# Kernel tuning notes

Measured on AMD Instinct MI355X. Metric: run time of the kernel, lower is better.

## Reference

```python
import jax, jax.numpy as jnp
import numpy as np

B, L, D = 2, 4096, 1024
H = 8
DK = D // H          # 128 head qk dim (expand_k=1)
DV = 2 * D // H      # 256 head v dim (expand_v=2)
FFN = 4 * D          # 4096
CHUNK = 64
EPS = 1e-6


def _ln(x, w, b):
    mu = x.mean(-1, keepdims=True)
    var = ((x - mu) ** 2).mean(-1, keepdims=True)
    return (x - mu) / jnp.sqrt(var + EPS) * w + b


def _retention(q, k, v):
    # q,k: [B,H,L,DK], v: [B,H,L,DV]; RetNet decayed causal linear attention,
    # computed chunkwise (intra-chunk parallel + inter-chunk recurrent state).
    Bq, Hq, Lq, Dk = q.shape
    Dv = v.shape[-1]
    N = Lq // CHUNK
    b = 1.0 - jnp.exp2(-5.0 - jnp.arange(Hq, dtype=q.dtype))   # [H] per-head decay
    logb = jnp.log(b)
    q = q * (Dk ** -0.5)
    t = jnp.arange(CHUNK, dtype=q.dtype)
    diff = t[:, None] - t[None, :]                              # [C,C]
    mask = jnp.where(diff >= 0, jnp.exp(logb[:, None, None] * diff), 0.0)  # [H,C,C]
    d_q = jnp.exp(logb[:, None] * (t[None, :] + 1.0))           # b^(t+1), [H,C]
    d_k = jnp.exp(logb[:, None] * (CHUNK - 1.0 - t[None, :]))   # b^(C-1-s), [H,C]
    d_c = jnp.exp(logb * CHUNK)                                 # b^C, [H]

    def to_chunks(x):
        return x.reshape(Bq, Hq, N, CHUNK, -1).transpose(2, 0, 1, 3, 4)  # [N,B,H,C,d]

    qc, kc, vc = to_chunks(q), to_chunks(k), to_chunks(v)
    S0 = jnp.zeros((Bq, Hq, Dk, Dv), q.dtype)

    def step(S, inp):
        qi, ki, vi = inp                                        # [B,H,C,*]
        A = jnp.einsum('bhtd,bhsd->bhts', qi, ki) * mask        # intra-chunk scores
        o = jnp.einsum('bhts,bhsv->bhtv', A, vi)
        o = o + jnp.einsum('bhtd,bhdv->bhtv', qi * d_q[None, :, :, None], S)
        S = S * d_c[None, :, None, None] + jnp.einsum('bhsd,bhsv->bhdv', ki * d_k[None, :, :, None], vi)
        return S, o

    _, os = jax.lax.scan(step, S0, (qc, kc, vc))                # os: [N,B,H,C,DV]
    return os.transpose(1, 2, 0, 3, 4).reshape(Bq, Hq, Lq, Dv)


def setup_inputs() -> dict:
    key = jax.random.key(0)
    ks = jax.random.split(key, 8)
    s = 0.02
    return {
        'x': jax.random.normal(ks[0], (B, L, D), jnp.float32),
        'ln1_w': jnp.ones((D,), jnp.float32),
        'ln1_b': jnp.zeros((D,), jnp.float32),
        'Wq': jax.random.normal(ks[1], (D, D), jnp.float32) * s,
        'Wk': jax.random.normal(ks[2], (D, D), jnp.float32) * s,
        'Wv': jax.random.normal(ks[3], (D, 2 * D), jnp.float32) * s,
        'Wo': jax.random.normal(ks[4], (2 * D, D), jnp.float32) * s,
        'ln2_w': jnp.ones((D,), jnp.float32),
        'ln2_b': jnp.zeros((D,), jnp.float32),
        'W1': jax.random.normal(ks[5], (D, FFN), jnp.float32) * s,
        'b1': jnp.zeros((FFN,), jnp.float32),
        'W2': jax.random.normal(ks[6], (FFN, D), jnp.float32) * s,
        'b2': jnp.zeros((D,), jnp.float32),
    }


def reference(x, ln1_w, ln1_b, Wq, Wk, Wv, Wo, ln2_w, ln2_b, W1, b1, W2, b2):
    # retention branch
    h = _ln(x, ln1_w, ln1_b)
    q = (h @ Wq).reshape(B, L, H, DK).transpose(0, 2, 1, 3)
    k = (h @ Wk).reshape(B, L, H, DK).transpose(0, 2, 1, 3)
    v = (h @ Wv).reshape(B, L, H, DV).transpose(0, 2, 1, 3)
    o = _retention(q, k, v)                                      # [B,H,L,DV]
    o = o.transpose(0, 2, 1, 3).reshape(B, L, H * DV)
    x = x + o @ Wo
    # FFN branch (exact gelu, no subln, eval-mode dropout)
    f = _ln(x, ln2_w, ln2_b)
    f = jax.nn.gelu(f @ W1 + b1, approximate=False)
    x = x + (f @ W2 + b2)
    return x
```

## Files before the change

### kernel.cpp

```cpp
#include <hip/hip_runtime.h>
#include <math.h>

typedef short s16;
typedef __attribute__((ext_vector_type(8))) short short8;
typedef __attribute__((ext_vector_type(4))) float f32x4;

__device__ __forceinline__ float bf2f_lo(unsigned u){ return __builtin_bit_cast(float, u << 16); }
__device__ __forceinline__ float bf2f_hi(unsigned u){ return __builtin_bit_cast(float, u & 0xffff0000u); }
__device__ __forceinline__ float bf2f(unsigned short h){ return __builtin_bit_cast(float, (unsigned)h << 16); }
__device__ __forceinline__ s16 f2bf(float f){
  unsigned u = __builtin_bit_cast(unsigned, f);
  u += 0x7fffu + ((u >> 16) & 1u);
  return (s16)(u >> 16);
}
__device__ __forceinline__ void unpack8(int4 v, float* f){
  unsigned a=(unsigned)v.x, b=(unsigned)v.y, c=(unsigned)v.z, d=(unsigned)v.w;
  f[0]=bf2f_lo(a); f[1]=bf2f_hi(a); f[2]=bf2f_lo(b); f[3]=bf2f_hi(b);
  f[4]=bf2f_lo(c); f[5]=bf2f_hi(c); f[6]=bf2f_lo(d); f[7]=bf2f_hi(d);
}
__device__ __forceinline__ void gl2lds16(const s16* g, s16* l){
  __builtin_amdgcn_global_load_lds((const __attribute__((address_space(1))) void*)g,
                                   (__attribute__((address_space(3))) void*)l, 16, 0, 0);
}

__global__ __launch_bounds__(256) void ln_bf16(const float* __restrict__ x,
                                               const float* __restrict__ w,
                                               const float* __restrict__ b,
                                               s16* __restrict__ out){
  int row = blockIdx.x; int t = threadIdx.x;
  const float* xr = x + (size_t)row * 1024;
  float4 v = *(const float4*)(xr + t*4);
  float s = v.x + v.y + v.z + v.w;
  float ss = v.x*v.x + v.y*v.y + v.z*v.z + v.w*v.w;
  for (int o = 32; o > 0; o >>= 1){ s += __shfl_down(s, o, 64); ss += __shfl_down(ss, o, 64); }
  __shared__ float red[8];
  int wid = t >> 6, lane = t & 63;
  if (lane == 0){ red[wid] = s; red[4+wid] = ss; }
  __syncthreads();
  if (t == 0){
    float S = red[0]+red[1]+red[2]+red[3];
    float SS = red[4]+red[5]+red[6]+red[7];
    red[0] = S * (1.f/1024.f);
    red[1] = SS * (1.f/1024.f);
  }
  __syncthreads();
  float mu = red[0];
  float var = red[1] - mu*mu;
  float rstd = rsqrtf(var + 1e-6f);
  float vv[4] = {v.x, v.y, v.z, v.w};
  short4 o4;
  s16 tmp[4];
  #pragma unroll
  for (int i = 0; i < 4; ++i){
    int c = t*4 + i;
    float val = (vv[i] - mu) * rstd * w[c] + b[c];
    tmp[i] = f2bf(val);
  }
  o4.x = tmp[0]; o4.y = tmp[1]; o4.z = tmp[2]; o4.w = tmp[3];
  *(short4*)(out + (size_t)row*1024 + t*4) = o4;
}

__global__ __launch_bounds__(256) void conv_t(const float* __restrict__ W,
                                              s16* __restrict__ Wt,
                                              int K, int N, float scale){
  __shared__ float tile[32][33];
  int n0 = blockIdx.x * 32, k0 = blockIdx.y * 32;
  int tx = threadIdx.x & 31, ty = threadIdx.x >> 5;
  #pragma unroll
  for (int i = 0; i < 4; ++i){
    int r = ty + i*8;
    tile[r][tx] = W[(size_t)(k0 + r)*N + n0 + tx];
  }
  __syncthreads();
  #pragma unroll
  for (int i = 0; i < 4; ++i){
    int r = ty + i*8;
    Wt[(size_t)(n0 + r)*K + k0 + tx] = f2bf(tile[tx][r] * scale);
  }
}

__device__ __forceinline__ void xcd_tile(int tiles_y, int& tx, int& ty){
  int id = blockIdx.x;
  int sy = tiles_y >> 3;
  int xcd = id & 7, p = id >> 3;
  ty = xcd * sy + (p % sy);
  tx = p / sy;
}

__global__ __launch_bounds__(512,2) void gemm256(const s16* __restrict__ A,
                                                 const s16* __restrict__ Bt,
                                                 int N, int K,
                                                 s16* __restrict__ Cb,
                                                 const float* __restrict__ bias,
                                                 int flags, int tiles_y){
  __shared__ s16 lds[2*4*8192];
  int t = threadIdx.x;
  int tx, ty; xcd_tile(tiles_y, tx, ty);
  int m0 = ty * 256, n0 = tx * 256;
  int w = t >> 6, lane = t & 63;
  int wm = w >> 2, wn = w & 3;
  int lrow = lane & 15, lq = lane >> 4;
  int s = lrow & 7;

  int grow = t >> 3;
  int g = (t & 7) ^ (grow & 7);
  const s16* Ag = A  + (size_t)(m0 + grow) * K + g*8;
  const s16* Bg = Bt + (size_t)(n0 + grow) * K + g*8;
  int wo = w * 512;

  int abase = (wm*64 + lrow) * 64;
  int bbase = (wn*32 + lrow) * 64;
  int sw0 = ((lq ^ s) << 3);
  int sw1 = (((4 + lq) ^ s) << 3);

  f32x4 acc[2][4][2][2];
  #pragma unroll
  for (int a = 0; a < 2; ++a)
    #pragma unroll
    for (int b = 0; b < 4; ++b)
      #pragma unroll
      for (int c = 0; c < 2; ++c)
        #pragma unroll
        for (int d = 0; d < 2; ++d) acc[a][b][c][d] = (f32x4){0.f,0.f,0.f,0.f};

  short8 af[2][4];
  short8 bfr[2][2][2];

#define STG_A(buf,h,kt) do{ \
    gl2lds16(Ag + (size_t)((h)*128    )*K + (kt)*64, lds + ((buf)*4+(h))*8192 + wo); \
    gl2lds16(Ag + (size_t)((h)*128+ 64)*K + (kt)*64, lds + ((buf)*4+(h))*8192 + 4096 + wo); }while(0)
#define STG_B(buf,nh,kt) do{ \
    gl2lds16(Bg + (size_t)((nh)*128    )*K + (kt)*64, lds + ((buf)*4+2+(nh))*8192 + wo); \
    gl2lds16(Bg + (size_t)((nh)*128+ 64)*K + (kt)*64, lds + ((buf)*4+2+(nh))*8192 + 4096 + wo); }while(0)
#define RD_A(buf,mh) do{ const s16* p_ = lds + ((buf)*4+(mh))*8192 + abase; \
    _Pragma("unroll") for (int m_ = 0; m_ < 4; ++m_){ \
      af[0][m_] = *(const short8*)(p_ + m_*1024 + sw0); \
      af[1][m_] = *(const short8*)(p_ + m_*1024 + sw1); } }while(0)
#define RD_B(buf,nh) do{ const s16* p_ = lds + ((buf)*4+2+(nh))*8192 + bbase; \
    _Pragma("unroll") for (int n_ = 0; n_ < 2; ++n_){ \
      bfr[nh][0][n_] = *(const short8*)(p_ + n_*1024 + sw0); \
      bfr[nh][1][n_] = *(const short8*)(p_ + n_*1024 + sw1); } }while(0)
#define MFMA_Q(mh,nh) do{ __builtin_amdgcn_s_setprio(1); \
    _Pragma("unroll") for (int kk_ = 0; kk_ < 2; ++kk_) \
      _Pragma("unroll") for (int m_ = 0; m_ < 4; ++m_) \
        _Pragma("unroll") for (int n_ = 0; n_ < 2; ++n_) \
          acc[mh][m_][nh][n_] = __builtin_amdgcn_mfma_f32_16x16x32_bf16( \
              af[kk_][m_], bfr[nh][kk_][n_], acc[mh][m_][nh][n_], 0, 0, 0); \
    __builtin_amdgcn_s_setprio(0); }while(0)
#define VM6() asm volatile("s_waitcnt vmcnt(6)" ::: "memory")
#define BARR() asm volatile("s_barrier" ::: "memory")

  int NT = K >> 6;
  STG_A(0,0,0); STG_B(0,0,0); STG_B(0,1,0); STG_A(0,1,0);

  for (int kt = 0; kt < NT-1; ++kt){
    int cb = kt & 1, nb = cb ^ 1;
    STG_A(nb,0,kt+1);
    VM6(); BARR();
    RD_A(cb,0); RD_B(cb,0);
    MFMA_Q(0,0);
    BARR();
    STG_B(nb,0,kt+1);
    VM6(); BARR();
    RD_B(cb,1);
    MFMA_Q(0,1);
    BARR();
    STG_B(nb,1,kt+1);
    VM6(); BARR();
    RD_A(cb,1);
    MFMA_Q(1,0);
    BARR();
    STG_A(nb,1,kt+1);
    BARR();
    MFMA_Q(1,1);
    BARR();
  }
  {
    int cb = (NT-1) & 1;
    asm volatile("s_waitcnt vmcnt(4)" ::: "memory"); BARR();
    RD_A(cb,0); RD_B(cb,0); MFMA_Q(0,0); BARR();
    asm volatile("s_waitcnt vmcnt(2)" ::: "memory"); BARR();
    RD_B(cb,1); MFMA_Q(0,1); BARR();
    asm volatile("s_waitcnt vmcnt(0)" ::: "memory"); BARR();
    RD_A(cb,1); MFMA_Q(1,0); BARR();
    MFMA_Q(1,1);
  }
#undef STG_A
#undef STG_B
#undef RD_A
#undef RD_B
#undef MFMA_Q
#undef VM6
#undef BARR

  bool do_gelu = flags & 1;
  #pragma unroll
  for (int nh = 0; nh < 2; ++nh){
    #pragma unroll
    for (int nj = 0; nj < 2; ++nj){
      int col = n0 + wn*32 + nh*128 + nj*16 + lrow;
      float bcol = bias ? bias[col] : 0.f;
      #pragma unroll
      for (int mh = 0; mh < 2; ++mh){
        #pragma unroll
        for (int m = 0; m < 4; ++m){
          int row_base = m0 + wm*64 + mh*128 + m*16 + lq*4;
          #pragma unroll
          for (int r = 0; r < 4; ++r){
            float val = acc[mh][m][nh][nj][r] + bcol;
            if (do_gelu) val = 0.5f * val * (1.f + erff(val * 0.70710678118654752f));
            Cb[(size_t)(row_base + r) * N + col] = f2bf(val);
          }
        }
      }
    }
  }
}

__global__ __launch_bounds__(256,2) void gemm_nt_h(const s16* __restrict__ A,
                                                   const s16* __restrict__ Bt,
                                                   int M, int N, int K, int ldb,
                                                   float* __restrict__ Cf,
                                                   s16* __restrict__ Cb,
                                                   const float* __restrict__ bias,
                                                   const float* __restrict__ resid,
                                                   int flags, int tiles_y){
  __shared__ s16 As0[64*32], As1[64*32];
  __shared__ s16 Bs0[128*32], Bs1[128*32];
  int t = threadIdx.x;
  int tx, ty; xcd_tile(tiles_y, tx, ty);
  int m0 = ty * 64, n0 = tx * 128;
  int w = t >> 6, lane = t & 63;
  int lrow = lane & 15, lq = lane >> 4;
  f32x4 acc[4][2];
  #pragma unroll
  for (int i = 0; i < 4; ++i)
    #pragma unroll
    for (int j = 0; j < 2; ++j) acc[i][j] = (f32x4){0.f,0.f,0.f,0.f};

  const s16* Ag = A  + (size_t)(m0 + (t>>2)) * K   + (t&3)*8;
  const s16* Bg = Bt + (size_t)(n0 + (t>>2)) * ldb + (t&3)*8;
  int wo = w*512;

  for (int k0 = 0; k0 < K; k0 += 64){
    __syncthreads();
    gl2lds16(Ag + k0,      As0 + wo);
    gl2lds16(Ag + k0 + 32, As1 + wo);
    gl2lds16(Bg + k0,                       Bs0 + wo);
    gl2lds16(Bg + (size_t)64*ldb + k0,      Bs0 + 2048 + wo);
    gl2lds16(Bg + k0 + 32,                  Bs1 + wo);
    gl2lds16(Bg + (size_t)64*ldb + k0 + 32, Bs1 + 2048 + wo);
    __syncthreads();
    short8 af[4], bfr[2];
    #pragma unroll
    for (int mi = 0; mi < 4; ++mi)
      af[mi] = *(short8*)&As0[(mi*16 + lrow)*32 + lq*8];
    #pragma unroll
    for (int ni = 0; ni < 2; ++ni)
      bfr[ni] = *(short8*)&Bs0[(w*32 + ni*16 + lrow)*32 + lq*8];
    #pragma unroll
    for (int mi = 0; mi < 4; ++mi)
      #pragma unroll
      for (int ni = 0; ni < 2; ++ni)
        acc[mi][ni] = __builtin_amdgcn_mfma_f32_16x16x32_bf16(af[mi], bfr[ni], acc[mi][ni], 0, 0, 0);
    #pragma unroll
    for (int mi = 0; mi < 4; ++mi)
      af[mi] = *(short8*)&As1[(mi*16 + lrow)*32 + lq*8];
    #pragma unroll
    for (int ni = 0; ni < 2; ++ni)
      bfr[ni] = *(short8*)&Bs1[(w*32 + ni*16 + lrow)*32 + lq*8];
    #pragma unroll
    for (int mi = 0; mi < 4; ++mi)
      #pragma unroll
      for (int ni = 0; ni < 2; ++ni)
        acc[mi][ni] = __builtin_amdgcn_mfma_f32_16x16x32_bf16(af[mi], bfr[ni], acc[mi][ni], 0, 0, 0);
  }

  bool do_gelu = flags & 1;
  bool out_bf = flags & 2;
  #pragma unroll
  for (int mi = 0; mi < 4; ++mi){
    #pragma unroll
    for (int ni = 0; ni < 2; ++ni){
      int gcol = n0 + w*32 + ni*16 + lrow;
      float bcol = bias ? bias[gcol] : 0.f;
      int grow_base = m0 + mi*16 + lq*4;
      #pragma unroll
      for (int r = 0; r < 4; ++r){
        int grow = grow_base + r;
        float val = acc[mi][ni][r] + bcol;
        if (do_gelu) val = 0.5f * val * (1.f + erff(val * 0.70710678118654752f));
        if (resid) val += resid[(size_t)grow * N + gcol];
        if (out_bf) Cb[(size_t)grow * N + gcol] = f2bf(val);
        else        Cf[(size_t)grow * N + gcol] = val;
      }
    }
  }
}

__global__ __launch_bounds__(256,2) void ret_chunksum(const s16* __restrict__ k,
                                                      const s16* __restrict__ v,
                                                      s16* __restrict__ U){
  int bi = blockIdx.x;
  int h = bi & 7, n = bi >> 3;
  int t = threadIdx.x;
  __shared__ s16 ks[128*72];
  __shared__ s16 vs[256*72];
  float log2b = log2f(1.f - exp2f(-5.f - (float)h));
  const s16* kbase = k + (size_t)(n*64)*4096 + h*128;
  const s16* vbase = v + (size_t)(n*64)*4096 + h*256;
  #pragma unroll
  for (int i = 0; i < 4; ++i){
    int e = i*2048 + t*8;
    int s = e >> 7, dk = e & 127;
    int4 kv = *(const int4*)(kbase + (size_t)s*4096 + dk);
    float f[8]; unpack8(kv, f);
    float dec = exp2f(log2b * (float)(63 - s));
    #pragma unroll
    for (int j = 0; j < 8; ++j) ks[(dk+j)*72 + s] = f2bf(f[j]*dec);
  }
  #pragma unroll
  for (int i = 0; i < 8; ++i){
    int e = i*2048 + t*8;
    int s = e >> 8, dv = e & 255;
    int4 vv = *(const int4*)(vbase + (size_t)s*4096 + dv);
    s16 tmp[8]; *(int4*)tmp = vv;
    #pragma unroll
    for (int j = 0; j < 8; ++j) vs[(dv+j)*72 + s] = tmp[j];
  }
  __syncthreads();
  int w = t >> 6, lane = t & 63;
  int m0w = w*64;
  int lrow = lane & 15, lq = lane >> 4;
  f32x4 acc[4][8];
  #pragma unroll
  for (int mi = 0; mi < 4; ++mi)
    #pragma unroll
    for (int ni = 0; ni < 8; ++ni) acc[mi][ni] = (f32x4){0.f,0.f,0.f,0.f};
  #pragma unroll
  for (int kk = 0; kk < 64; kk += 32){
    short8 af[4], bfr[8];
    #pragma unroll
    for (int mi = 0; mi < 4; ++mi)
      af[mi] = *(short8*)&vs[(m0w + mi*16 + lrow)*72 + kk + lq*8];
    #pragma unroll
    for (int ni = 0; ni < 8; ++ni)
      bfr[ni] = *(short8*)&ks[(ni*16 + lrow)*72 + kk + lq*8];
    #pragma unroll
    for (int mi = 0; mi < 4; ++mi)
      #pragma unroll
      for (int ni = 0; ni < 8; ++ni)
        acc[mi][ni] = __builtin_amdgcn_mfma_f32_16x16x32_bf16(af[mi], bfr[ni], acc[mi][ni], 0, 0, 0);
  }
  s16* Ub = U + ((size_t)(h*64 + n))*32768;
  #pragma unroll
  for (int mi = 0; mi < 4; ++mi)
    #pragma unroll
    for (int ni = 0; ni < 8; ++ni)
      #pragma unroll
      for (int r = 0; r < 4; ++r){
        int row = m0w + mi*16 + lq*4 + r;
        int col = ni*16 + lrow;
        Ub[(size_t)row*128 + col] = f2bf(acc[mi][ni][r]);
      }
}

__global__ __launch_bounds__(256) void ret_scan(s16* __restrict__ US){
  int tid = blockIdx.x*256 + threadIdx.x;
  int h = tid >> 12;
  int rem = tid & 4095;
  int dv = rem >> 4, dk0 = (rem & 15)*8;
  float log2b = log2f(1.f - exp2f(-5.f - (float)h));
  float dc = exp2f(log2b * 64.f);
  s16* base = US + (size_t)h*64*32768 + (size_t)dv*128 + dk0;
  float acc[8] = {0.f,0.f,0.f,0.f,0.f,0.f,0.f,0.f};
  #pragma unroll 4
  for (int n = 0; n < 64; ++n){
    s16* p = base + (size_t)n*32768;
    int4 u4 = *(const int4*)p;
    float uf[8]; unpack8(u4, uf);
    s16 sb[8];
    #pragma unroll
    for (int j = 0; j < 8; ++j) sb[j] = f2bf(acc[j]);
    *(int4*)p = *(int4*)sb;
    #pragma unroll
    for (int j = 0; j < 8; ++j) acc[j] = acc[j]*dc + uf[j];
  }
}

__global__ __launch_bounds__(256,2) void ret_attn(const s16* __restrict__ q,
                                                  const s16* __restrict__ k,
                                                  const s16* __restrict__ v,
                                                  const s16* __restrict__ S,
                                                  s16* __restrict__ o){
  int bi = blockIdx.x;
  int h = bi & 7, n = bi >> 3;
  int t = threadIdx.x;
  int w = t >> 6, lane = t & 63;
  int lrow = lane & 15, lq = lane >> 4;
  float log2b = log2f(1.f - exp2f(-5.f - (float)h));
  __shared__ s16 As[64*72];
  __shared__ s16 vs[256*72];

  const s16* vbase = v + (size_t)(n*64)*4096 + h*256;
  #pragma unroll
  for (int i = 0; i < 8; ++i){
    int e = i*2048 + t*8;
    int s = e >> 8, dv = e & 255;
    int4 vv = *(const int4*)(vbase + (size_t)s*4096 + dv);
    s16 tmp[8]; *(int4*)tmp = vv;
    #pragma unroll
    for (int j = 0; j < 8; ++j) vs[(dv+j)*72 + s] = tmp[j];
  }

  const s16* qbase = q + (size_t)(n*64)*4096 + h*128;
  const s16* kbase = k + (size_t)(n*64)*4096 + h*128;
  short8 qf[4][4];
  #pragma unroll
  for (int ti = 0; ti < 4; ++ti)
    #pragma unroll
    for (int c = 0; c < 4; ++c)
      qf[ti][c] = *(const short8*)(qbase + (size_t)(ti*16 + lrow)*4096 + c*32 + lq*8);
  short8 kf[4];
  #pragma unroll
  for (int c = 0; c < 4; ++c)
    kf[c] = *(const short8*)(kbase + (size_t)(16*w + lrow)*4096 + c*32 + lq*8);
  #pragma unroll
  for (int ti = 0; ti < 4; ++ti){
    f32x4 acc_a = (f32x4){0.f,0.f,0.f,0.f};
    #pragma unroll
    for (int c = 0; c < 4; ++c)
      acc_a = __builtin_amdgcn_mfma_f32_16x16x32_bf16(qf[ti][c], kf[c], acc_a, 0, 0, 0);
    #pragma unroll
    for (int r = 0; r < 4; ++r){
      int ti_idx = ti*16 + lq*4 + r;
      int s_idx = 16*w + lrow;
      int d = ti_idx - s_idx;
      float val = (d >= 0) ? acc_a[r] * exp2f(log2b * (float)d) : 0.f;
      As[ti_idx*72 + s_idx] = f2bf(val);
    }
  }
  __syncthreads();

  f32x4 acc[4][4];
  #pragma unroll
  for (int mi = 0; mi < 4; ++mi)
    #pragma unroll
    for (int nj = 0; nj < 4; ++nj) acc[mi][nj] = (f32x4){0.f,0.f,0.f,0.f};

  const s16* Sbase = S + ((size_t)(h*64 + n)*256 + w*64)*128;
  #pragma unroll
  for (int c = 0; c < 4; ++c){
    short8 bf[4];
    #pragma unroll
    for (int nj = 0; nj < 4; ++nj)
      bf[nj] = *(const short8*)(Sbase + (size_t)(nj*16 + lrow)*128 + c*32 + lq*8);
    #pragma unroll
    for (int mi = 0; mi < 4; ++mi)
      #pragma unroll
      for (int nj = 0; nj < 4; ++nj)
        acc[mi][nj] = __builtin_amdgcn_mfma_f32_16x16x32_bf16(qf[mi][c], bf[nj], acc[mi][nj], 0, 0, 0);
  }
  #pragma unroll
  for (int mi = 0; mi < 4; ++mi){
    #pragma unroll
    for (int r = 0; r < 4; ++r){
      float dq = exp2f(log2b * (float)(mi*16 + lq*4 + r + 1));
      #pragma unroll
      for (int nj = 0; nj < 4; ++nj) acc[mi][nj][r] *= dq;
    }
  }
  #pragma unroll
  for (int c = 0; c < 2; ++c){
    short8 af[4], bf[4];
    #pragma unroll
    for (int mi = 0; mi < 4; ++mi)
      af[mi] = *(short8*)&As[(mi*16 + lrow)*72 + c*32 + lq*8];
    #pragma unroll
    for (int nj = 0; nj < 4; ++nj)
      bf[nj] = *(short8*)&vs[(w*64 + nj*16 + lrow)*72 + c*32 + lq*8];
    #pragma unroll
    for (int mi = 0; mi < 4; ++mi)
      #pragma unroll
      for (int nj = 0; nj < 4; ++nj)
        acc[mi][nj] = __builtin_amdgcn_mfma_f32_16x16x32_bf16(af[mi], bf[nj], acc[mi][nj], 0, 0, 0);
  }
  s16* obase = o + (size_t)(n*64)*2048 + h*256;
  #pragma unroll
  for (int mi = 0; mi < 4; ++mi)
    #pragma unroll
    for (int nj = 0; nj < 4; ++nj)
      #pragma unroll
      for (int r = 0; r < 4; ++r){
        int row = mi*16 + lq*4 + r;
        int col = w*64 + nj*16 + lrow;
        obase[(size_t)row*2048 + col] = f2bf(acc[mi][nj][r]);
      }
}

extern "C" void kernel_launch(void* const* d_in, const int* in_sizes, int n_in,
                              void* d_out, int out_size, void* d_ws, size_t ws_size,
                              hipStream_t stream) {
  (void)in_sizes; (void)n_in; (void)out_size; (void)ws_size;
  const float* x     = (const float*)d_in[0];
  const float* ln1_w = (const float*)d_in[1];
  const float* ln1_b = (const float*)d_in[2];
  const float* Wq    = (const float*)d_in[3];
  const float* Wk    = (const float*)d_in[4];
  const float* Wv    = (const float*)d_in[5];
  const float* Wo    = (const float*)d_in[6];
  const float* ln2_w = (const float*)d_in[7];
  const float* ln2_b = (const float*)d_in[8];
  const float* W1    = (const float*)d_in[9];
  const float* b1    = (const float*)d_in[10];
  const float* W2    = (const float*)d_in[11];
  const float* b2    = (const float*)d_in[12];
  float* out = (float*)d_out;
  char* ws = (char*)d_ws;

  const size_t MB = 1ull << 20;
  s16* Wqkv_t = (s16*)(ws + 0*MB);
  s16* Wo_t = (s16*)(ws + 8*MB);
  s16* W1_t = (s16*)(ws + 12*MB);
  s16* W2_t = (s16*)(ws + 20*MB);
  s16* hbuf = (s16*)(ws + 28*MB);
  s16* h2   = (s16*)(ws + 28*MB);
  s16* qkv  = (s16*)(ws + 44*MB);
  float* x1 = (float*)(ws + 44*MB);
  s16* fb   = (s16*)(ws + 76*MB);
  s16* US   = (s16*)(ws + 108*MB);
  s16* ob   = (s16*)(ws + 140*MB);

  conv_t<<<dim3(32,32),  256, 0, stream>>>(Wq, Wqkv_t, 1024, 1024, 0.08838834764831845f);
  conv_t<<<dim3(32,32),  256, 0, stream>>>(Wk, Wqkv_t + (size_t)1024*1024, 1024, 1024, 1.f);
  conv_t<<<dim3(64,32),  256, 0, stream>>>(Wv, Wqkv_t + (size_t)2048*1024, 1024, 2048, 1.f);
  conv_t<<<dim3(32,64),  256, 0, stream>>>(Wo, Wo_t, 2048, 1024, 1.f);
  conv_t<<<dim3(128,32), 256, 0, stream>>>(W1, W1_t, 1024, 4096, 1.f);
  conv_t<<<dim3(32,128), 256, 0, stream>>>(W2, W2_t, 4096, 1024, 1.f);

  ln_bf16<<<8192, 256, 0, stream>>>(x, ln1_w, ln1_b, hbuf);

  gemm256<<<512, 512, 0, stream>>>(hbuf, Wqkv_t, 4096, 1024, qkv, nullptr, 0, 32);

  for (int b = 0; b < 2; ++b){
    const s16* q_b = qkv + (size_t)b*4096*4096;
    const s16* k_b = q_b + 1024;
    const s16* v_b = q_b + 2048;
    s16* ob_b = ob + (size_t)b*4096*2048;
    ret_chunksum<<<512, 256, 0, stream>>>(k_b, v_b, US);
    ret_scan<<<128, 256, 0, stream>>>(US);
    ret_attn<<<512, 256, 0, stream>>>(q_b, k_b, v_b, US, ob_b);
  }

  gemm_nt_h<<<1024, 256, 0, stream>>>(ob, Wo_t, 8192, 1024, 2048, 2048, x1, nullptr, nullptr, x, 0, 128);
  ln_bf16<<<8192, 256, 0, stream>>>(x1, ln2_w, ln2_b, h2);

  gemm256<<<512, 512, 0, stream>>>(h2, W1_t, 4096, 1024, fb, b1, 1, 32);
  gemm_nt_h<<<1024, 256, 0, stream>>>(fb, W2_t, 8192, 1024, 4096, 4096, out, nullptr, b2, x1, 0, 128);
}
```

Measured before the change: 623.1 us.

## Deepen gemm256 prefetch pipeline and replace narrow-N GEMM with 256x128 pipelined kernel

The gemm256 main loop now prefetches two k-tiles ahead, issuing loads for the next-next tile into the buffer just consumed, so global-to-LDS latency overlaps more MFMA work. A new gemm256h kernel (256x128 tiles, 512 threads, swizzled LDS, same staged pipeline) replaces the small 64x128 gemm_nt_h for the Wo and W2 projections. The aim is higher data reuse and fewer launched blocks per output. The cost is more LDS per block and only 256 blocks, which may underfill the CUs.

```diff
diff --git a/kernel.cpp b/kernel.cpp
--- a/kernel.cpp
+++ b/kernel.cpp
@@ -86,6 +86,9 @@
   ty = xcd * sy + (p % sy);
   tx = p / sy;
 }
+
+#define VMW(n) asm volatile("s_waitcnt vmcnt(" #n ")" ::: "memory")
+#define BARR() asm volatile("s_barrier" ::: "memory")
 
 __global__ __launch_bounds__(512,2) void gemm256(const s16* __restrict__ A,
                                                  const s16* __restrict__ Bt,
@@ -147,42 +150,47 @@
           acc[mh][m_][nh][n_] = __builtin_amdgcn_mfma_f32_16x16x32_bf16( \
               af[kk_][m_], bfr[nh][kk_][n_], acc[mh][m_][nh][n_], 0, 0, 0); \
     __builtin_amdgcn_s_setprio(0); }while(0)
-#define VM6() asm volatile("s_waitcnt vmcnt(6)" ::: "memory")
-#define BARR() asm volatile("s_barrier" ::: "memory")
 
   int NT = K >> 6;
   STG_A(0,0,0); STG_B(0,0,0); STG_B(0,1,0); STG_A(0,1,0);
-
-  for (int kt = 0; kt < NT-1; ++kt){
+  STG_A(1,0,1); STG_B(1,0,1); STG_B(1,1,1);
+  VMW(6); BARR();
+
+  for (int kt = 0; kt < NT-2; ++kt){
     int cb = kt & 1, nb = cb ^ 1;
-    STG_A(nb,0,kt+1);
-    VM6(); BARR();
     RD_A(cb,0); RD_B(cb,0);
-    MFMA_Q(0,0);
-    BARR();
-    STG_B(nb,0,kt+1);
-    VM6(); BARR();
+    STG_A(nb,1,kt+1);
+    BARR(); MFMA_Q(0,0); BARR();
     RD_B(cb,1);
-    MFMA_Q(0,1);
-    BARR();
-    STG_B(nb,1,kt+1);
-    VM6(); BARR();
+    STG_A(cb,0,kt+2);
+    BARR(); MFMA_Q(0,1); BARR();
     RD_A(cb,1);
-    MFMA_Q(1,0);
-    BARR();
-    STG_A(nb,1,kt+1);
-    BARR();
-    MFMA_Q(1,1);
-    BARR();
+    STG_B(cb,0,kt+2);
+    BARR(); MFMA_Q(1,0); BARR();
+    STG_B(cb,1,kt+2);
+    VMW(6);
+    BARR(); MFMA_Q(1,1); BARR();
+  }
+  {
+    int cb = (NT-2) & 1, nb = cb ^ 1;
+    RD_A(cb,0); RD_B(cb,0);
+    STG_A(nb,1,NT-1);
+    BARR(); MFMA_Q(0,0); BARR();
+    RD_B(cb,1);
+    BARR(); MFMA_Q(0,1); BARR();
+    RD_A(cb,1);
+    BARR(); MFMA_Q(1,0); BARR();
+    VMW(0);
+    BARR(); MFMA_Q(1,1); BARR();
   }
   {
     int cb = (NT-1) & 1;
-    asm volatile("s_waitcnt vmcnt(4)" ::: "memory"); BARR();
-    RD_A(cb,0); RD_B(cb,0); MFMA_Q(0,0); BARR();
-    asm volatile("s_waitcnt vmcnt(2)" ::: "memory"); BARR();
-    RD_B(cb,1); MFMA_Q(0,1); BARR();
-    asm volatile("s_waitcnt vmcnt(0)" ::: "memory"); BARR();
-    RD_A(cb,1); MFMA_Q(1,0); BARR();
+    RD_A(cb,0); RD_B(cb,0);
+    BARR(); MFMA_Q(0,0); BARR();
+    RD_B(cb,1);
+    BARR(); MFMA_Q(0,1); BARR();
+    RD_A(cb,1);
+    BARR(); MFMA_Q(1,0); BARR();
     MFMA_Q(1,1);
   }
 #undef STG_A
@@ -190,8 +198,6 @@
 #undef RD_A
 #undef RD_B
 #undef MFMA_Q
-#undef VM6
-#undef BARR
 
   bool do_gelu = flags & 1;
   #pragma unroll
@@ -217,82 +223,123 @@
   }
 }
 
-__global__ __launch_bounds__(256,2) void gemm_nt_h(const s16* __restrict__ A,
-                                                   const s16* __restrict__ Bt,
-                                                   int M, int N, int K, int ldb,
-                                                   float* __restrict__ Cf,
-                                                   s16* __restrict__ Cb,
-                                                   const float* __restrict__ bias,
-                                                   const float* __restrict__ resid,
-                                                   int flags, int tiles_y){
-  __shared__ s16 As0[64*32], As1[64*32];
-  __shared__ s16 Bs0[128*32], Bs1[128*32];
+__global__ __launch_bounds__(512,2) void gemm256h(const s16* __restrict__ A,
+                                                  const s16* __restrict__ Bt,
+                                                  int N, int K,
+                                                  float* __restrict__ Cf,
+                                                  s16* __restrict__ Cb,
+                                                  const float* __restrict__ bias,
+                                                  const float* __restrict__ resid,
+                                                  int flags, int tiles_y){
+  __shared__ s16 lds[2*3*8192];
   int t = threadIdx.x;
   int tx, ty; xcd_tile(tiles_y, tx, ty);
-  int m0 = ty * 64, n0 = tx * 128;
+  int m0 = ty * 256, n0 = tx * 128;
   int w = t >> 6, lane = t & 63;
+  int wm = w >> 2, wn = w & 3;
   int lrow = lane & 15, lq = lane >> 4;
-  f32x4 acc[4][2];
-  #pragma unroll
-  for (int i = 0; i < 4; ++i)
-    #pragma unroll
-    for (int j = 0; j < 2; ++j) acc[i][j] = (f32x4){0.f,0.f,0.f,0.f};
-
-  const s16* Ag = A  + (size_t)(m0 + (t>>2)) * K   + (t&3)*8;
-  const s16* Bg = Bt + (size_t)(n0 + (t>>2)) * ldb + (t&3)*8;
-  int wo = w*512;
-
-  for (int k0 = 0; k0 < K; k0 += 64){
-    __syncthreads();
-    gl2lds16(Ag + k0,      As0 + wo);
-    gl2lds16(Ag + k0 + 32, As1 + wo);
-    gl2lds16(Bg + k0,                       Bs0 + wo);
-    gl2lds16(Bg + (size_t)64*ldb + k0,      Bs0 + 2048 + wo);
-    gl2lds16(Bg + k0 + 32,                  Bs1 + wo);
-    gl2lds16(Bg + (size_t)64*ldb + k0 + 32, Bs1 + 2048 + wo);
-    __syncthreads();
-    short8 af[4], bfr[2];
-    #pragma unroll
-    for (int mi = 0; mi < 4; ++mi)
-      af[mi] = *(short8*)&As0[(mi*16 + lrow)*32 + lq*8];
-    #pragma unroll
-    for (int ni = 0; ni < 2; ++ni)
-      bfr[ni] = *(short8*)&Bs0[(w*32 + ni*16 + lrow)*32 + lq*8];
-    #pragma unroll
-    for (int mi = 0; mi < 4; ++mi)
-      #pragma unroll
-      for (int ni = 0; ni < 2; ++ni)
-        acc[mi][ni] = __builtin_amdgcn_mfma_f32_16x16x32_bf16(af[mi], bfr[ni], acc[mi][ni], 0, 0, 0);
-    #pragma unroll
-    for (int mi = 0; mi < 4; ++mi)
-      af[mi] = *(short8*)&As1[(mi*16 + lrow)*32 + lq*8];
-    #pragma unroll
-    for (int ni = 0; ni < 2; ++ni)
-      bfr[ni] = *(short8*)&Bs1[(w*32 + ni*16 + lrow)*32 + lq*8];
-    #pragma unroll
-    for (int mi = 0; mi < 4; ++mi)
-      #pragma unroll
-      for (int ni = 0; ni < 2; ++ni)
-        acc[mi][ni] = __builtin_amdgcn_mfma_f32_16x16x32_bf16(af[mi], bfr[ni], acc[mi][ni], 0, 0, 0);
-  }
+  int s = lrow & 7;
+
+  int grow = t >> 3;
+  int g = (t & 7) ^ (grow & 7);
+  const s16* Ag = A  + (size_t)(m0 + grow) * K + g*8;
+  const s16* Bg = Bt + (size_t)(n0 + grow) * K + g*8;
+  int wo = w * 512;
+
+  int abase = (wm*64 + lrow) * 64;
+  int bbase = (wn*32 + lrow) * 64;
+  int sw0 = ((lq ^ s) << 3);
+  int sw1 = (((4 + lq) ^ s) << 3);
+
+  f32x4 acc[2][4][2];
+  #pragma unroll
+  for (int a = 0; a < 2; ++a)
+    #pragma unroll
+    for (int b = 0; b < 4; ++b)
+      #pragma unroll
+      for (int c = 0; c < 2; ++c) acc[a][b][c] = (f32x4){0.f,0.f,0.f,0.f};
+
+  short8 af[2][4], bfr[2][2];
+
+#define STG_A(buf,h,kt) do{ \
+    gl2lds16(Ag + (size_t)((h)*128    )*K + (kt)*64, lds + ((buf)*3+(h))*8192 + wo); \
+    gl2lds16(Ag + (size_t)((h)*128+ 64)*K + (kt)*64, lds + ((buf)*3+(h))*8192 + 4096 + wo); }while(0)
+#define STG_B(buf,kt) do{ \
+    gl2lds16(Bg + (size_t)0*K  + (kt)*64, lds + ((buf)*3+2)*8192 + wo); \
+    gl2lds16(Bg + (size_t)64*K + (kt)*64, lds + ((buf)*3+2)*8192 + 4096 + wo); }while(0)
+#define RD_A(buf,mh) do{ const s16* p_ = lds + ((buf)*3+(mh))*8192 + abase; \
+    _Pragma("unroll") for (int m_ = 0; m_ < 4; ++m_){ \
+      af[0][m_] = *(const short8*)(p_ + m_*1024 + sw0); \
+      af[1][m_] = *(const short8*)(p_ + m_*1024 + sw1); } }while(0)
+#define RD_B(buf) do{ const s16* p_ = lds + ((buf)*3+2)*8192 + bbase; \
+    _Pragma("unroll") for (int n_ = 0; n_ < 2; ++n_){ \
+      bfr[0][n_] = *(const short8*)(p_ + n_*1024 + sw0); \
+      bfr[1][n_] = *(const short8*)(p_ + n_*1024 + sw1); } }while(0)
+#define MFMA_H(mh) do{ __builtin_amdgcn_s_setprio(1); \
+    _Pragma("unroll") for (int kk_ = 0; kk_ < 2; ++kk_) \
+      _Pragma("unroll") for (int m_ = 0; m_ < 4; ++m_) \
+        _Pragma("unroll") for (int n_ = 0; n_ < 2; ++n_) \
+          acc[mh][m_][n_] = __builtin_amdgcn_mfma_f32_16x16x32_bf16( \
+              af[kk_][m_], bfr[kk_][n_], acc[mh][m_][n_], 0, 0, 0); \
+    __builtin_amdgcn_s_setprio(0); }while(0)
+
+  int NT = K >> 6;
+  STG_A(0,0,0); STG_B(0,0); STG_A(0,1,0);
+  STG_A(1,0,1); STG_B(1,1);
+  VMW(4); BARR();
+
+  for (int kt = 0; kt < NT-2; ++kt){
+    int cb = kt & 1, nb = cb ^ 1;
+    RD_A(cb,0); RD_B(cb);
+    STG_A(nb,1,kt+1);
+    BARR(); MFMA_H(0); BARR();
+    RD_A(cb,1);
+    STG_A(cb,0,kt+2); STG_B(cb,kt+2);
+    VMW(4);
+    BARR(); MFMA_H(1); BARR();
+  }
+  {
+    int cb = (NT-2) & 1, nb = cb ^ 1;
+    RD_A(cb,0); RD_B(cb);
+    STG_A(nb,1,NT-1);
+    BARR(); MFMA_H(0); BARR();
+    RD_A(cb,1);
+    VMW(0);
+    BARR(); MFMA_H(1); BARR();
+  }
+  {
+    int cb = (NT-1) & 1;
+    RD_A(cb,0); RD_B(cb);
+    BARR(); MFMA_H(0); BARR();
+    RD_A(cb,1);
+    MFMA_H(1);
+  }
+#undef STG_A
+#undef STG_B
+#undef RD_A
+#undef RD_B
+#undef MFMA_H
 
   bool do_gelu = flags & 1;
   bool out_bf = flags & 2;
   #pragma unroll
-  for (int mi = 0; mi < 4; ++mi){
-    #pragma unroll
-    for (int ni = 0; ni < 2; ++ni){
-      int gcol = n0 + w*32 + ni*16 + lrow;
-      float bcol = bias ? bias[gcol] : 0.f;
-      int grow_base = m0 + mi*16 + lq*4;
-      #pragma unroll
-      for (int r = 0; r < 4; ++r){
-        int grow = grow_base + r;
-        float val = acc[mi][ni][r] + bcol;
-        if (do_gelu) val = 0.5f * val * (1.f + erff(val * 0.70710678118654752f));
-        if (resid) val += resid[(size_t)grow * N + gcol];
-        if (out_bf) Cb[(size_t)grow * N + gcol] = f2bf(val);
-        else        Cf[(size_t)grow * N + gcol] = val;
+  for (int nj = 0; nj < 2; ++nj){
+    int col = n0 + wn*32 + nj*16 + lrow;
+    float bcol = bias ? bias[col] : 0.f;
+    #pragma unroll
+    for (int mh = 0; mh < 2; ++mh){
+      #pragma unroll
+      for (int m = 0; m < 4; ++m){
+        int row_base = m0 + wm*64 + mh*128 + m*16 + lq*4;
+        #pragma unroll
+        for (int r = 0; r < 4; ++r){
+          int grow_ = row_base + r;
+          float val = acc[mh][m][nj][r] + bcol;
+          if (do_gelu) val = 0.5f * val * (1.f + erff(val * 0.70710678118654752f));
+          if (resid) val += resid[(size_t)grow_ * N + col];
+          if (out_bf) Cb[(size_t)grow_ * N + col] = f2bf(val);
+          else        Cf[(size_t)grow_ * N + col] = val;
+        }
       }
     }
   }
@@ -552,9 +599,9 @@
     ret_attn<<<512, 256, 0, stream>>>(q_b, k_b, v_b, US, ob_b);
   }
 
-  gemm_nt_h<<<1024, 256, 0, stream>>>(ob, Wo_t, 8192, 1024, 2048, 2048, x1, nullptr, nullptr, x, 0, 128);
+  gemm256h<<<256, 512, 0, stream>>>(ob, Wo_t, 1024, 2048, x1, nullptr, nullptr, x, 0, 32);
   ln_bf16<<<8192, 256, 0, stream>>>(x1, ln2_w, ln2_b, h2);
 
   gemm256<<<512, 512, 0, stream>>>(h2, W1_t, 4096, 1024, fb, b1, 1, 32);
-  gemm_nt_h<<<1024, 256, 0, stream>>>(fb, W2_t, 8192, 1024, 4096, 4096, out, nullptr, b2, x1, 0, 128);
-}
+  gemm256h<<<256, 512, 0, stream>>>(fb, W2_t, 1024, 4096, out, nullptr, b2, x1, 0, 32);
+}
```

New measurement: 604.4 us. -3.0%, faster.
